# Optimization experiments

Measured on AMD Instinct MI355X. Metric: run time of the kernel, lower is better.

The kernel has to match this reference:

```python
import jax, jax.numpy as jnp
import numpy as np

P = 16            # patch_size
D = 256           # hidden_dim == P*P (required by final reshape)
H = 8             # num_heads
HD = D // H       # head_dim


def _sinusoid(n, d):
    # standard sinusoidal positional encoding, interleaved sin/cos
    pos = jnp.arange(n, dtype=jnp.float32)[:, None]            # (n,1)
    i = jnp.arange(0, d, 2, dtype=jnp.float32)                 # (d/2,)
    div = jnp.exp(-i * (jnp.log(10000.0) / d))                 # (d/2,)
    ang = pos * div                                            # (n, d/2)
    return jnp.stack([jnp.sin(ang), jnp.cos(ang)], axis=-1).reshape(n, d)


def _patch_embed(x, w, b):
    # Conv2d(in_ch, D, kernel=P, stride=P) then flatten to (B, N, D)
    e = jax.lax.conv_general_dilated(
        x, w, window_strides=(P, P), padding='VALID',
        dimension_numbers=('NCHW', 'OIHW', 'NCHW'))
    e = e + b[None, :, None, None]
    B = e.shape[0]
    e = e.reshape(B, D, -1).transpose(0, 2, 1)                 # (B, N, D)
    e = e + _sinusoid(e.shape[1], D)[None]                     # positional enc
    return e.reshape(B, -1, H, HD).transpose(0, 2, 1, 3)       # (B, H, N, HD)


def setup_inputs() -> dict:
    key = jax.random.key(0)
    ks = jax.random.split(key, 12)
    B = 16
    inp = {
        'q': jax.random.normal(ks[0], (B, 3, 512, 512), jnp.float32),
        'k': jax.random.normal(ks[1], (B, 3, 512, 512), jnp.float32),
        'v': jax.random.normal(ks[2], (B, 3, 512, 512), jnp.float32),
        'a': jax.random.normal(ks[3], (B, 3, 256, 256), jnp.float32),
    }
    s = 0.02
    for idx, name in enumerate('qkva'):
        inp['w' + name] = jax.random.normal(ks[4 + 2 * idx], (D, 3, P, P), jnp.float32) * s
        inp['b' + name] = jnp.zeros((D,), jnp.float32)
    return inp


def reference(q, k, v, a, wq, bq, wk, bk, wv, bv, wa, ba):
    qh = _patch_embed(q, wq, bq)   # (B,H,Nq,HD), Nq=1024
    kh = _patch_embed(k, wk, bk)   # (B,H,Nk,HD)
    vh = _patch_embed(v, wv, bv)   # (B,H,Nk,HD)
    ah = _patch_embed(a, wa, ba)   # (B,H,Na,HD), Na=256
    scale = HD ** -0.5
    # agent attention: two small softmax matmuls then Q @ (K @ V)
    Qs = jax.nn.softmax(jnp.einsum('bhnd,bhmd->bhnm', qh, ah) * scale, axis=-1)  # (B,H,Nq,Na)
    Ks = jax.nn.softmax(jnp.einsum('bhmd,bhnd->bhmn', ah, kh) * scale, axis=-1)  # (B,H,Na,Nk)
    KV = jnp.einsum('bhmn,bhnd->bhmd', Ks, vh)                                   # (B,H,Na,HD)
    A = jnp.einsum('bhnm,bhmd->bhnd', Qs, KV)                                    # (B,H,Nq,HD)
    B = A.shape[0]
    attn = A.transpose(0, 2, 1, 3).reshape(B, -1, D)            # (B, Nq, D)
    N = attn.shape[1]
    g = int(N ** 0.5)                                           # grid side (32)
    HW = g * P                                                  # 512
    attn = attn.reshape(B, N, P, P)
    attn = attn.reshape(B, g, g, P, P).transpose(0, 1, 3, 2, 4).reshape(B, HW, HW)
    return attn
```

## Files before the change

### kernel.cpp

```cpp
#include <hip/hip_runtime.h>
#include <cstdint>
#include <cstddef>

typedef __bf16 bf16x8 __attribute__((ext_vector_type(8)));
typedef float f32x4 __attribute__((ext_vector_type(4)));
typedef unsigned short u16x4 __attribute__((ext_vector_type(4)));
typedef unsigned short u16x8 __attribute__((ext_vector_type(8)));

#define MFMA16(a, b, c) __builtin_amdgcn_mfma_f32_16x16x32_bf16(a, b, c, 0, 0, 0)

__device__ __forceinline__ unsigned short f2bf(float f) {
    unsigned u = __builtin_bit_cast(unsigned, f);
    u = (u + 0x7FFFu + ((u >> 16) & 1u)) >> 16;
    return (unsigned short)u;
}

__global__ void pe_fill(float* __restrict__ pe) {
    int n = blockIdx.x;
    int d = threadIdx.x;
    int j = d >> 1;
    float div = expf(-(float)(2 * j) * 0.03597789207808881f);
    float ang = (float)n * div;
    pe[n * 256 + d] = (d & 1) ? cosf(ang) : sinf(ang);
}

struct EmbedArgs {
    const float* src;
    const float* W;
    const float* bias;
    const float* pe;
    unsigned short* dst;
    int Np, lgNp, G, lgG, imgS, trans;
};

__global__ __launch_bounds__(512)
void embed_all(EmbedArgs A0, EmbedArgs A1, EmbedArgs A2, EmbedArgs A3) {
    __shared__ unsigned short As[128][40];
    __shared__ unsigned short Bs[256][40];

    const int bx = blockIdx.x;
    EmbedArgs A;
    if      (bx < 128) A = A0;
    else if (bx < 256) A = A1;
    else if (bx < 384) A = A2;
    else               A = A3;
    const int m0 = (bx & 127) * 128;

    const int t = threadIdx.x;
    const int lane = t & 63, wid = t >> 6;
    const int wr = wid >> 2, wc = wid & 3;
    const int l15 = lane & 15, l4 = lane >> 4;

    int arow[2], akq[2];
    const float* abase[2];
#pragma unroll
    for (int i = 0; i < 2; ++i) {
        int f = t + i * 512;
        arow[i] = f >> 3;
        akq[i] = (f & 7) * 4;
        int m = m0 + arow[i];
        int b = m >> A.lgNp, n = m & (A.Np - 1);
        int gy = n >> A.lgG, gx = n & (A.G - 1);
        abase[i] = A.src + ((size_t)(b * 3) * A.imgS + gy * 16) * (size_t)A.imgS + gx * 16;
    }
    int bcol[4], bkq[4];
#pragma unroll
    for (int i = 0; i < 4; ++i) {
        int f = t + i * 512;
        bcol[i] = f >> 3;
        bkq[i] = (f & 7) * 4;
    }

    f32x4 acc[4][4];
#pragma unroll
    for (int i = 0; i < 4; ++i)
#pragma unroll
        for (int j = 0; j < 4; ++j) acc[i][j] = f32x4{0.f, 0.f, 0.f, 0.f};

    for (int k0 = 0; k0 < 768; k0 += 32) {
        f32x4 av[2], bv[4];
#pragma unroll
        for (int i = 0; i < 2; ++i) {
            int k = k0 + akq[i];
            int c = k >> 8, py = (k >> 4) & 15, px = k & 15;
            av[i] = *(const f32x4*)(abase[i] + ((size_t)c * A.imgS + py) * (size_t)A.imgS + px);
        }
#pragma unroll
        for (int i = 0; i < 4; ++i)
            bv[i] = *(const f32x4*)(A.W + (size_t)bcol[i] * 768 + k0 + bkq[i]);

        __syncthreads();
#pragma unroll
        for (int i = 0; i < 2; ++i) {
            u16x4 o;
#pragma unroll
            for (int j = 0; j < 4; ++j) o[j] = f2bf(av[i][j]);
            *(u16x4*)&As[arow[i]][akq[i]] = o;
        }
#pragma unroll
        for (int i = 0; i < 4; ++i) {
            u16x4 o;
#pragma unroll
            for (int j = 0; j < 4; ++j) o[j] = f2bf(bv[i][j]);
            *(u16x4*)&Bs[bcol[i]][bkq[i]] = o;
        }
        __syncthreads();

        bf16x8 af[4], bfr[4];
#pragma unroll
        for (int m16 = 0; m16 < 4; ++m16)
            af[m16] = *(const bf16x8*)&As[wr * 64 + m16 * 16 + l15][l4 * 8];
#pragma unroll
        for (int n16 = 0; n16 < 4; ++n16)
            bfr[n16] = *(const bf16x8*)&Bs[wc * 64 + n16 * 16 + l15][l4 * 8];
#pragma unroll
        for (int m16 = 0; m16 < 4; ++m16)
#pragma unroll
            for (int n16 = 0; n16 < 4; ++n16)
                acc[m16][n16] = MFMA16(af[m16], bfr[n16], acc[m16][n16]);
    }

#pragma unroll
    for (int m16 = 0; m16 < 4; ++m16) {
#pragma unroll
        for (int n16 = 0; n16 < 4; ++n16) {
            int d = wc * 64 + n16 * 16 + l15;
            int hh = d >> 5, hd = d & 31;
            float bsv = A.bias[d];
#pragma unroll
            for (int r = 0; r < 4; ++r) {
                int row = wr * 64 + m16 * 16 + l4 * 4 + r;
                int m = m0 + row;
                int b = m >> A.lgNp, n = m & (A.Np - 1);
                float v = acc[m16][n16][r] + bsv + A.pe[n * 256 + d];
                unsigned short bvv = f2bf(v);
                if (A.trans)
                    A.dst[(((size_t)(b * 8 + hh)) * 32 + hd) * (size_t)A.Np + n] = bvv;
                else
                    A.dst[(((size_t)(b * 8 + hh)) * (size_t)A.Np + n) * 32 + hd] = bvv;
            }
        }
    }
}

__global__ __launch_bounds__(512)
void s2kv_kernel(const unsigned short* __restrict__ ah_ws,
                 const unsigned short* __restrict__ kh_ws,
                 const unsigned short* __restrict__ vT_ws,
                 unsigned short* __restrict__ kvT_ws) {
    __shared__ unsigned short ahs[128][40];
    __shared__ unsigned short khs[128][40];
    __shared__ unsigned short vts[32][136];
    __shared__ unsigned short Ps[128][136];

    const int bid = blockIdx.x;
    const int half = bid & 1;
    const int h = (bid >> 1) & 7, b = bid >> 4;
    const int a0 = half * 128;
    const int t = threadIdx.x, lane = t & 63, wid = t >> 6;
    const int l15 = lane & 15, l4 = lane >> 4;
    const size_t bh = (size_t)(b * 8 + h);

    const unsigned short* ahp = ah_ws + (bh * 256 + a0) * 32;
    const unsigned short* khp = kh_ws + bh * 1024 * 32;
    const unsigned short* vtp = vT_ws + bh * 32 * 1024;

    {
        int row = t >> 2, kq = (t & 3) * 8;
        *(u16x8*)&ahs[row][kq] = *(const u16x8*)(ahp + row * 32 + kq);
    }
    __syncthreads();
    const bf16x8 af = *(const bf16x8*)&ahs[wid * 16 + l15][l4 * 8];

    const float scale = 0.17677669529663687f;
    float rs[4] = {0.f, 0.f, 0.f, 0.f};
    const f32x4 z = {0.f, 0.f, 0.f, 0.f};
    f32x4 kv[2];
    kv[0] = z; kv[1] = z;

    for (int kt = 0; kt < 8; ++kt) {
        const int n0 = kt * 128;
        __syncthreads();
        {
            int row = t >> 2, kq = (t & 3) * 8;
            *(u16x8*)&khs[row][kq] = *(const u16x8*)(khp + (size_t)(n0 + row) * 32 + kq);
        }
        {
            int row = t >> 4, cq = (t & 15) * 8;
            *(u16x8*)&vts[row][cq] = *(const u16x8*)(vtp + (size_t)row * 1024 + n0 + cq);
        }
        __syncthreads();
#pragma unroll
        for (int n16 = 0; n16 < 8; ++n16) {
            bf16x8 bfr = *(const bf16x8*)&khs[n16 * 16 + l15][l4 * 8];
            f32x4 s = MFMA16(af, bfr, z);
#pragma unroll
            for (int r = 0; r < 4; ++r) {
                float e = __expf(s[r] * scale);
                rs[r] += e;
                Ps[wid * 16 + l4 * 4 + r][n16 * 16 + l15] = f2bf(e);
            }
        }
        __syncthreads();
#pragma unroll
        for (int ks = 0; ks < 4; ++ks) {
            bf16x8 pa = *(const bf16x8*)&Ps[wid * 16 + l15][ks * 32 + l4 * 8];
#pragma unroll
            for (int n16 = 0; n16 < 2; ++n16) {
                bf16x8 vb = *(const bf16x8*)&vts[n16 * 16 + l15][ks * 32 + l4 * 8];
                kv[n16] = MFMA16(pa, vb, kv[n16]);
            }
        }
    }
#pragma unroll
    for (int r = 0; r < 4; ++r) {
        rs[r] += __shfl_xor(rs[r], 1, 64);
        rs[r] += __shfl_xor(rs[r], 2, 64);
        rs[r] += __shfl_xor(rs[r], 4, 64);
        rs[r] += __shfl_xor(rs[r], 8, 64);
    }
#pragma unroll
    for (int n16 = 0; n16 < 2; ++n16)
#pragma unroll
        for (int r = 0; r < 4; ++r) {
            int m = a0 + wid * 16 + l4 * 4 + r;
            int d = n16 * 16 + l15;
            kvT_ws[bh * 8192 + (size_t)d * 256 + m] = f2bf(kv[n16][r] / rs[r]);
        }
}

__global__ __launch_bounds__(256)
void qsa_kernel(const unsigned short* __restrict__ qh_ws,
                const unsigned short* __restrict__ ah_ws,
                const unsigned short* __restrict__ kvT_ws,
                float* __restrict__ out) {
    __shared__ unsigned short qhs[64][40];
    __shared__ unsigned short ahs[256][40];
    __shared__ unsigned short kvt[32][264];
    __shared__ unsigned short Ps[64][264];

    const int bid = blockIdx.x;
    const int qt = bid & 15, h = (bid >> 4) & 7, b = bid >> 7;
    const int m0 = qt * 64;
    const int t = threadIdx.x, lane = t & 63, wid = t >> 6;
    const int l15 = lane & 15, l4 = lane >> 4;
    const size_t bh = (size_t)(b * 8 + h);

    const unsigned short* qhp = qh_ws + (bh * 1024 + m0) * 32;
    const unsigned short* ahp = ah_ws + bh * 256 * 32;

    {
        int row = t >> 2, kq = (t & 3) * 8;
        *(u16x8*)&qhs[row][kq] = *(const u16x8*)(qhp + row * 32 + kq);
    }
    {
        *(u16x8*)&ahs[t][0]  = *(const u16x8*)(ahp + (size_t)t * 32);
        *(u16x8*)&ahs[t][8]  = *(const u16x8*)(ahp + (size_t)t * 32 + 8);
        *(u16x8*)&ahs[t][16] = *(const u16x8*)(ahp + (size_t)t * 32 + 16);
        *(u16x8*)&ahs[t][24] = *(const u16x8*)(ahp + (size_t)t * 32 + 24);
    }
#pragma unroll
    for (int i = 0; i < 4; ++i) {
        int chunk = t + i * 256;
        int row = chunk >> 5, cq = (chunk & 31) * 8;
        *(u16x8*)&kvt[row][cq] = *(const u16x8*)(kvT_ws + bh * 8192 + (size_t)row * 256 + cq);
    }
    __syncthreads();

    const bf16x8 qa = *(const bf16x8*)&qhs[wid * 16 + l15][l4 * 8];
    const float scale = 0.17677669529663687f;
    const f32x4 z = {0.f, 0.f, 0.f, 0.f};
    float rs[4] = {0.f, 0.f, 0.f, 0.f};
#pragma unroll
    for (int n16 = 0; n16 < 16; ++n16) {
        bf16x8 bfr = *(const bf16x8*)&ahs[n16 * 16 + l15][l4 * 8];
        f32x4 s = MFMA16(qa, bfr, z);
#pragma unroll
        for (int r = 0; r < 4; ++r) {
            float e = __expf(s[r] * scale);
            rs[r] += e;
            Ps[wid * 16 + l4 * 4 + r][n16 * 16 + l15] = f2bf(e);
        }
    }
#pragma unroll
    for (int r = 0; r < 4; ++r) {
        rs[r] += __shfl_xor(rs[r], 1, 64);
        rs[r] += __shfl_xor(rs[r], 2, 64);
        rs[r] += __shfl_xor(rs[r], 4, 64);
        rs[r] += __shfl_xor(rs[r], 8, 64);
    }
    __syncthreads();

    f32x4 o[2];
    o[0] = z; o[1] = z;
#pragma unroll
    for (int ks = 0; ks < 8; ++ks) {
        bf16x8 pa = *(const bf16x8*)&Ps[wid * 16 + l15][ks * 32 + l4 * 8];
#pragma unroll
        for (int n16 = 0; n16 < 2; ++n16) {
            bf16x8 kb = *(const bf16x8*)&kvt[n16 * 16 + l15][ks * 32 + l4 * 8];
            o[n16] = MFMA16(pa, kb, o[n16]);
        }
    }
#pragma unroll
    for (int n16 = 0; n16 < 2; ++n16) {
#pragma unroll
        for (int r = 0; r < 4; ++r) {
            int row = wid * 16 + l4 * 4 + r;
            int n = m0 + row;
            int gy = n >> 5, gx = n & 31;
            int hd = n16 * 16 + l15;
            int py = 2 * h + (hd >> 4), px = hd & 15;
            out[((size_t)b * 512 + gy * 16 + py) * 512 + gx * 16 + px] = o[n16][r] / rs[r];
        }
    }
}

extern "C" void kernel_launch(void* const* d_in, const int* in_sizes, int n_in,
                              void* d_out, int out_size, void* d_ws, size_t ws_size,
                              hipStream_t stream) {
    (void)in_sizes; (void)n_in; (void)out_size; (void)ws_size;

    const float* q  = (const float*)d_in[0];
    const float* k  = (const float*)d_in[1];
    const float* v  = (const float*)d_in[2];
    const float* a  = (const float*)d_in[3];
    const float* wq = (const float*)d_in[4];
    const float* bq = (const float*)d_in[5];
    const float* wk = (const float*)d_in[6];
    const float* bk = (const float*)d_in[7];
    const float* wv = (const float*)d_in[8];
    const float* bv = (const float*)d_in[9];
    const float* wa = (const float*)d_in[10];
    const float* ba = (const float*)d_in[11];
    float* out = (float*)d_out;

    char* ws = (char*)d_ws;
    float* pe           = (float*)(ws);
    unsigned short* qh  = (unsigned short*)(ws + 1048576);
    unsigned short* kh  = (unsigned short*)(ws + 9437184);
    unsigned short* ah  = (unsigned short*)(ws + 17825792);
    unsigned short* vT  = (unsigned short*)(ws + 19922944);
    unsigned short* kvT = (unsigned short*)(ws + 28311552);

    pe_fill<<<1024, 256, 0, stream>>>(pe);

    EmbedArgs Aq = { q, wq, bq, pe, qh, 1024, 10, 32, 5, 512, 0 };
    EmbedArgs Ak = { k, wk, bk, pe, kh, 1024, 10, 32, 5, 512, 0 };
    EmbedArgs Av = { v, wv, bv, pe, vT, 1024, 10, 32, 5, 512, 1 };
    EmbedArgs Aa = { a, wa, ba, pe, ah,  256,  8, 16, 4, 256, 0 };
    embed_all<<<416, 512, 0, stream>>>(Aq, Ak, Av, Aa);

    s2kv_kernel<<<256, 512, 0, stream>>>(ah, kh, vT, kvT);
    qsa_kernel<<<2048, 256, 0, stream>>>(qh, ah, kvT, out);
}
```

Before: 102.9 us.

## Pre-pack weights to bf16 MFMA layout and drop LDS staging in patch embed

Result: slower. 126.6 us (+23.0%).

```diff
diff --git a/kernel.cpp b/kernel.cpp
--- a/kernel.cpp
+++ b/kernel.cpp
@@ -3,6 +3,7 @@
 #include <cstddef>
 
 typedef __bf16 bf16x8 __attribute__((ext_vector_type(8)));
+typedef __bf16 bf16x4 __attribute__((ext_vector_type(4)));
 typedef float f32x4 __attribute__((ext_vector_type(4)));
 typedef unsigned short u16x4 __attribute__((ext_vector_type(4)));
 typedef unsigned short u16x8 __attribute__((ext_vector_type(8)));
@@ -15,61 +16,62 @@
     return (unsigned short)u;
 }
 
-__global__ void pe_fill(float* __restrict__ pe) {
-    int n = blockIdx.x;
-    int d = threadIdx.x;
-    int j = d >> 1;
-    float div = expf(-(float)(2 * j) * 0.03597789207808881f);
-    float ang = (float)n * div;
-    pe[n * 256 + d] = (d & 1) ? cosf(ang) : sinf(ang);
-}
-
-struct EmbedArgs {
+__global__ __launch_bounds__(256)
+void prep(float* __restrict__ pe, unsigned short* __restrict__ Wb,
+          const float* __restrict__ w0, const float* __restrict__ w1,
+          const float* __restrict__ w2, const float* __restrict__ w3) {
+    const int bx = blockIdx.x, t = threadIdx.x;
+    if (bx < 1024) {
+        int n = bx, d = t;
+        int j = d >> 1;
+        float div = expf(-(float)(2 * j) * 0.03597789207808881f);
+        float ang = (float)n * div;
+        pe[n * 256 + d] = (d & 1) ? cosf(ang) : sinf(ang);
+    } else {
+        int i = bx - 1024;
+        int tensor = i / 192, blk = i - tensor * 192;
+        const float* w = (tensor == 0) ? w0 : (tensor == 1) ? w1 : (tensor == 2) ? w2 : w3;
+        int idx4 = blk * 256 + t;
+        int d = idx4 / 192;
+        int kq = (idx4 - d * 192) * 4;
+        f32x4 v = *(const f32x4*)(w + (size_t)idx4 * 4);
+        u16x4 o;
+#pragma unroll
+        for (int e = 0; e < 4; ++e) o[e] = f2bf(v[e]);
+        unsigned short* dst = Wb + (size_t)tensor * 196608
+                            + (d >> 4) * 12288 + (kq >> 5) * 512
+                            + (d & 15) * 32 + (kq & 31);
+        *(u16x4*)dst = o;
+    }
+}
+
+struct EArgs {
     const float* src;
-    const float* W;
+    const unsigned short* Wb;
     const float* bias;
     const float* pe;
     unsigned short* dst;
-    int Np, lgNp, G, lgG, imgS, trans;
+    int Np, lgNp, lgG, S, trans;
 };
 
-__global__ __launch_bounds__(512)
-void embed_all(EmbedArgs A0, EmbedArgs A1, EmbedArgs A2, EmbedArgs A3) {
-    __shared__ unsigned short As[128][40];
-    __shared__ unsigned short Bs[256][40];
-
-    const int bx = blockIdx.x;
-    EmbedArgs A;
-    if      (bx < 128) A = A0;
-    else if (bx < 256) A = A1;
-    else if (bx < 384) A = A2;
-    else               A = A3;
-    const int m0 = (bx & 127) * 128;
-
-    const int t = threadIdx.x;
-    const int lane = t & 63, wid = t >> 6;
-    const int wr = wid >> 2, wc = wid & 3;
+template<bool TR>
+__device__ __forceinline__ void embed_body(const EArgs& A, int m0) {
+    const int t = threadIdx.x, lane = t & 63, wid = t >> 6;
     const int l15 = lane & 15, l4 = lane >> 4;
-
-    int arow[2], akq[2];
-    const float* abase[2];
-#pragma unroll
-    for (int i = 0; i < 2; ++i) {
-        int f = t + i * 512;
-        arow[i] = f >> 3;
-        akq[i] = (f & 7) * 4;
-        int m = m0 + arow[i];
-        int b = m >> A.lgNp, n = m & (A.Np - 1);
-        int gy = n >> A.lgG, gx = n & (A.G - 1);
-        abase[i] = A.src + ((size_t)(b * 3) * A.imgS + gy * 16) * (size_t)A.imgS + gx * 16;
-    }
-    int bcol[4], bkq[4];
-#pragma unroll
-    for (int i = 0; i < 4; ++i) {
-        int f = t + i * 512;
-        bcol[i] = f >> 3;
-        bkq[i] = (f & 7) * 4;
-    }
+    const int S = A.S;
+
+    const float* pbase[4];
+    int nn[4], bb[4];
+#pragma unroll
+    for (int j = 0; j < 4; ++j) {
+        int p = m0 + j * 16 + l15;
+        int b = p >> A.lgNp, n = p & (A.Np - 1);
+        nn[j] = n; bb[j] = b;
+        int gy = n >> A.lgG, gx = n & ((1 << A.lgG) - 1);
+        pbase[j] = A.src + ((size_t)(b * 3) * S + gy * 16 + (l4 >> 1)) * (size_t)S
+                 + gx * 16 + (l4 & 1) * 8;
+    }
+    const unsigned short* wbase = A.Wb + (size_t)(wid * 4) * 12288 + l15 * 32 + l4 * 8;
 
     f32x4 acc[4][4];
 #pragma unroll
@@ -77,70 +79,77 @@
 #pragma unroll
         for (int j = 0; j < 4; ++j) acc[i][j] = f32x4{0.f, 0.f, 0.f, 0.f};
 
-    for (int k0 = 0; k0 < 768; k0 += 32) {
-        f32x4 av[2], bv[4];
-#pragma unroll
-        for (int i = 0; i < 2; ++i) {
-            int k = k0 + akq[i];
-            int c = k >> 8, py = (k >> 4) & 15, px = k & 15;
-            av[i] = *(const f32x4*)(abase[i] + ((size_t)c * A.imgS + py) * (size_t)A.imgS + px);
+    for (int kt = 0; kt < 24; ++kt) {
+        const size_t aoff = ((size_t)(kt >> 3) * S + (kt & 7) * 2) * (size_t)S;
+        bf16x8 pf[4], wf[4];
+#pragma unroll
+        for (int j = 0; j < 4; ++j) {
+            f32x4 lo = *(const f32x4*)(pbase[j] + aoff);
+            f32x4 hi = *(const f32x4*)(pbase[j] + aoff + 4);
+            bf16x8 v;
+#pragma unroll
+            for (int e = 0; e < 4; ++e) { v[e] = (__bf16)lo[e]; v[4 + e] = (__bf16)hi[e]; }
+            pf[j] = v;
         }
 #pragma unroll
         for (int i = 0; i < 4; ++i)
-            bv[i] = *(const f32x4*)(A.W + (size_t)bcol[i] * 768 + k0 + bkq[i]);
-
-        __syncthreads();
-#pragma unroll
-        for (int i = 0; i < 2; ++i) {
-            u16x4 o;
-#pragma unroll
-            for (int j = 0; j < 4; ++j) o[j] = f2bf(av[i][j]);
-            *(u16x4*)&As[arow[i]][akq[i]] = o;
-        }
+            wf[i] = *(const bf16x8*)(wbase + i * 12288 + kt * 512);
+#pragma unroll
+        for (int i = 0; i < 4; ++i)
+#pragma unroll
+            for (int j = 0; j < 4; ++j) {
+                if (TR) acc[i][j] = MFMA16(pf[i], wf[j], acc[i][j]);
+                else    acc[i][j] = MFMA16(wf[i], pf[j], acc[i][j]);
+            }
+    }
+
+    if (!TR) {
 #pragma unroll
         for (int i = 0; i < 4; ++i) {
-            u16x4 o;
-#pragma unroll
-            for (int j = 0; j < 4; ++j) o[j] = f2bf(bv[i][j]);
-            *(u16x4*)&Bs[bcol[i]][bkq[i]] = o;
-        }
-        __syncthreads();
-
-        bf16x8 af[4], bfr[4];
-#pragma unroll
-        for (int m16 = 0; m16 < 4; ++m16)
-            af[m16] = *(const bf16x8*)&As[wr * 64 + m16 * 16 + l15][l4 * 8];
-#pragma unroll
-        for (int n16 = 0; n16 < 4; ++n16)
-            bfr[n16] = *(const bf16x8*)&Bs[wc * 64 + n16 * 16 + l15][l4 * 8];
-#pragma unroll
-        for (int m16 = 0; m16 < 4; ++m16)
-#pragma unroll
-            for (int n16 = 0; n16 < 4; ++n16)
-                acc[m16][n16] = MFMA16(af[m16], bfr[n16], acc[m16][n16]);
-    }
-
-#pragma unroll
-    for (int m16 = 0; m16 < 4; ++m16) {
-#pragma unroll
-        for (int n16 = 0; n16 < 4; ++n16) {
-            int d = wc * 64 + n16 * 16 + l15;
+            int d0 = wid * 64 + i * 16 + l4 * 4;
+            int hh = d0 >> 5, hd = d0 & 31;
+            f32x4 bs = *(const f32x4*)&A.bias[d0];
+#pragma unroll
+            for (int j = 0; j < 4; ++j) {
+                int n = nn[j], b = bb[j];
+                f32x4 pv = *(const f32x4*)&A.pe[n * 256 + d0];
+                bf16x4 o;
+#pragma unroll
+                for (int r = 0; r < 4; ++r)
+                    o[r] = (__bf16)(acc[i][j][r] + bs[r] + pv[r]);
+                *(bf16x4*)&A.dst[(((size_t)(b * 8 + hh)) * A.Np + n) * 32 + hd] = o;
+            }
+        }
+    } else {
+#pragma unroll
+        for (int j = 0; j < 4; ++j) {
+            int d = wid * 64 + j * 16 + l15;
             int hh = d >> 5, hd = d & 31;
             float bsv = A.bias[d];
 #pragma unroll
-            for (int r = 0; r < 4; ++r) {
-                int row = wr * 64 + m16 * 16 + l4 * 4 + r;
-                int m = m0 + row;
-                int b = m >> A.lgNp, n = m & (A.Np - 1);
-                float v = acc[m16][n16][r] + bsv + A.pe[n * 256 + d];
-                unsigned short bvv = f2bf(v);
-                if (A.trans)
-                    A.dst[(((size_t)(b * 8 + hh)) * 32 + hd) * (size_t)A.Np + n] = bvv;
-                else
-                    A.dst[(((size_t)(b * 8 + hh)) * (size_t)A.Np + n) * 32 + hd] = bvv;
-            }
-        }
-    }
+            for (int i = 0; i < 4; ++i) {
+                int p0 = m0 + i * 16 + l4 * 4;
+                int b = p0 >> A.lgNp, n0 = p0 & (A.Np - 1);
+                bf16x4 o;
+#pragma unroll
+                for (int r = 0; r < 4; ++r)
+                    o[r] = (__bf16)(acc[i][j][r] + bsv + A.pe[(n0 + r) * 256 + d]);
+                *(bf16x4*)&A.dst[(((size_t)(b * 8 + hh)) * 32 + hd) * (size_t)A.Np + n0] = o;
+            }
+        }
+    }
+}
+
+__global__ __launch_bounds__(256, 3)
+void embed2(EArgs A0, EArgs A1, EArgs A2, EArgs A3) {
+    const int bx = blockIdx.x;
+    EArgs A; int m0;
+    if      (bx < 256) { A = A0; m0 = bx * 64; }
+    else if (bx < 512) { A = A1; m0 = (bx - 256) * 64; }
+    else if (bx < 768) { A = A2; m0 = (bx - 512) * 64; }
+    else               { A = A3; m0 = (bx - 768) * 64; }
+    if (A.trans) embed_body<true>(A, m0);
+    else         embed_body<false>(A, m0);
 }
 
 __global__ __launch_bounds__(512)
@@ -337,19 +346,20 @@
 
     char* ws = (char*)d_ws;
     float* pe           = (float*)(ws);
-    unsigned short* qh  = (unsigned short*)(ws + 1048576);
-    unsigned short* kh  = (unsigned short*)(ws + 9437184);
-    unsigned short* ah  = (unsigned short*)(ws + 17825792);
-    unsigned short* vT  = (unsigned short*)(ws + 19922944);
-    unsigned short* kvT = (unsigned short*)(ws + 28311552);
-
-    pe_fill<<<1024, 256, 0, stream>>>(pe);
-
-    EmbedArgs Aq = { q, wq, bq, pe, qh, 1024, 10, 32, 5, 512, 0 };
-    EmbedArgs Ak = { k, wk, bk, pe, kh, 1024, 10, 32, 5, 512, 0 };
-    EmbedArgs Av = { v, wv, bv, pe, vT, 1024, 10, 32, 5, 512, 1 };
-    EmbedArgs Aa = { a, wa, ba, pe, ah,  256,  8, 16, 4, 256, 0 };
-    embed_all<<<416, 512, 0, stream>>>(Aq, Ak, Av, Aa);
+    unsigned short* Wb  = (unsigned short*)(ws + 1048576);
+    unsigned short* kvT = (unsigned short*)(ws);
+    unsigned short* qh  = (unsigned short*)(ws + 2621440);
+    unsigned short* kh  = (unsigned short*)(ws + 11010048);
+    unsigned short* ah  = (unsigned short*)(ws + 19398656);
+    unsigned short* vT  = (unsigned short*)(ws + 21495808);
+
+    prep<<<1792, 256, 0, stream>>>(pe, Wb, wq, wk, wv, wa);
+
+    EArgs Aq = { q, Wb,              bq, pe, qh, 1024, 10, 5, 512, 0 };
+    EArgs Ak = { k, Wb + 196608,     bk, pe, kh, 1024, 10, 5, 512, 0 };
+    EArgs Av = { v, Wb + 2 * 196608, bv, pe, vT, 1024, 10, 5, 512, 1 };
+    EArgs Aa = { a, Wb + 3 * 196608, ba, pe, ah,  256,  8, 4, 256, 0 };
+    embed2<<<832, 256, 0, stream>>>(Aq, Ak, Av, Aa);
 
     s2kv_kernel<<<256, 512, 0, stream>>>(ah, kh, vT, kvT);
     qsa_kernel<<<2048, 256, 0, stream>>>(qh, ah, kvT, out);
```
